# Kernel tuning notes

Measured on AMD Instinct MI355X. Metric: run time of the kernel, lower is better.

## Reference

```python
import jax, jax.numpy as jnp
import numpy as np


def setup_inputs() -> dict:
    key = jax.random.key(0)
    k1, k2 = jax.random.split(key)
    z = jax.random.normal(k1, (16, 128, 32, 32), dtype=jnp.float32)
    e = jax.random.normal(k2, (8192, 128), dtype=jnp.float32)
    log_sigma = jnp.zeros((1,), dtype=jnp.float32)  # init_log_sigma = 0.0
    return {"z": z, "e": e, "log_sigma": log_sigma}


def reference(z, e, log_sigma):
    # z: [B, C, H, W] latents; e: [M, C] codebook; log_sigma: [1]
    B, C, H, W = z.shape
    zf = jnp.transpose(z, (0, 2, 3, 1)).reshape(-1, C)  # [N, C]
    N = zf.shape[0]
    M = e.shape[0]
    T = 1.0  # latent_temp default

    # squared L2 distance via expanded dot products: ||z||^2 + ||e||^2 - 2 z.e
    z_sq = jnp.sum(zf * zf, axis=1, keepdims=True)          # [N, 1]
    e_sq = jnp.sum(e * e, axis=1)[None, :]                  # [1, M]
    dist = jnp.maximum(z_sq + e_sq - 2.0 * (zf @ e.T), 0.0)  # [N, M]

    alpha = -1.0 / (2.0 * jnp.exp(log_sigma[0]) ** 2)
    A = alpha * dist / T                                     # [N, M]

    # np.log(np.e) == 1.0 in the original
    const = 0.5 * C * (2.0 * log_sigma - 1.0)                # [1]
    lse1_loss = -jnp.mean(T * jax.nn.logsumexp(A, axis=1)) + const + jnp.log(float(M))
    lse2_loss = -jnp.mean(T * jax.nn.logsumexp(A, axis=0)) + const + jnp.log(float(N))
    return lse1_loss, lse2_loss
```

## Files before the change

### kernel.cpp

```cpp
#include <hip/hip_runtime.h>
#include <hip/hip_bf16.h>

typedef unsigned short u16;
typedef __attribute__((ext_vector_type(8))) short short8;
typedef __attribute__((ext_vector_type(4))) float float4v;

#define N_ROWS 16384
#define M_COLS 8192
#define KDIM   128
#define SHIFT  64.0f
#define STRIPES 64
#define SPLITS  32
#define CHUNKS  4

__device__ inline u16 f2bf(float f) {
  unsigned u = __builtin_bit_cast(unsigned, f);
  unsigned r = (u + 0x7fffu + ((u >> 16) & 1u)) >> 16;
  return (u16)r;
}

__global__ void prep(const float* __restrict__ z, const float* __restrict__ e,
                     u16* __restrict__ zf, u16* __restrict__ ef,
                     float* __restrict__ zsq, float* __restrict__ esq,
                     double* __restrict__ dacc, unsigned* __restrict__ dcnt) {
  if (blockIdx.x < 512) {
    const int b = blockIdx.x >> 5, h = blockIdx.x & 31;
    __shared__ float tile[128 * 33];
    __shared__ float psum[8][32];
    const float* src = z + ((size_t)b * 128 * 32 + h) * 32;
    for (int idx = threadIdx.x; idx < 4096; idx += 256) {
      int c = idx >> 5, w = idx & 31;
      tile[c * 33 + w] = src[c * 1024 + w];
    }
    __syncthreads();
    {
      int w = threadIdx.x & 31, cg = threadIdx.x >> 5;
      float s = 0.f;
#pragma unroll
      for (int cc = 0; cc < 16; ++cc) {
        float v = tile[(cg * 16 + cc) * 33 + w];
        s = fmaf(v, v, s);
      }
      psum[cg][w] = s;
    }
    for (int idx = threadIdx.x; idx < 512; idx += 256) {
      int w = idx >> 4, g = idx & 15;
      short8 v;
#pragma unroll
      for (int cc = 0; cc < 8; ++cc) v[cc] = (short)f2bf(tile[(g * 8 + cc) * 33 + w]);
      *(short8*)&zf[((size_t)b * 1024 + h * 32 + w) * 128 + g * 8] = v;
    }
    __syncthreads();
    if (threadIdx.x < 32) {
      int w = threadIdx.x;
      float s = 0.f;
#pragma unroll
      for (int cg = 0; cg < 8; ++cg) s += psum[cg][w];
      zsq[b * 1024 + h * 32 + w] = s;
    }
  } else {
    if (blockIdx.x == 512 && threadIdx.x == 0) {
      __hip_atomic_store(&dacc[0], 0.0, __ATOMIC_RELAXED, __HIP_MEMORY_SCOPE_AGENT);
      __hip_atomic_store(&dacc[1], 0.0, __ATOMIC_RELAXED, __HIP_MEMORY_SCOPE_AGENT);
      __hip_atomic_store(dcnt, 0u, __ATOMIC_RELAXED, __HIP_MEMORY_SCOPE_AGENT);
    }
    const int gw = ((blockIdx.x - 512) * 256 + threadIdx.x) >> 6;
    const int ln = threadIdx.x & 63;
    for (int r = gw; r < M_COLS; r += 512) {
      float2 v = *(const float2*)&e[r * 128 + ln * 2];
      unsigned pk = (unsigned)f2bf(v.x) | ((unsigned)f2bf(v.y) << 16);
      *(unsigned*)&ef[r * 128 + ln * 2] = pk;
      float s = fmaf(v.x, v.x, v.y * v.y);
#pragma unroll
      for (int sh = 1; sh < 64; sh <<= 1) s += __shfl_xor(s, sh);
      if (ln == 0) esq[r] = s;
    }
  }
}

__global__ __launch_bounds__(512, 4) void gemm_lse(
    const u16* __restrict__ zf, const u16* __restrict__ ef,
    const float* __restrict__ zsq, const float* __restrict__ esq,
    const float* __restrict__ log_sigma,
    float* __restrict__ rpart, float* __restrict__ cpart) {
  __shared__ __align__(16) u16 et[256 * 128];
  __shared__ float colacc[8][256];
  const int tid = threadIdx.x;
  const int ln = tid & 63, wv = tid >> 6;
  const int l15 = ln & 15, q = ln >> 4;
  const int stripe = blockIdx.x, split = blockIdx.y;
  const int colbase = split * 256;

  {
    const u16* efb = ef + (size_t)colbase * 128;
#pragma unroll
    for (int it = 0; it < 8; ++it) {
      int u = it * 512 + tid;
      int r = u >> 4, p_ = u & 15;
      int g = p_ ^ (r & 15);
      __builtin_amdgcn_global_load_lds(
          (const __attribute__((address_space(1))) unsigned int*)(efb + r * 128 + g * 8),
          (__attribute__((address_space(3))) unsigned int*)(et + (it * 512 + wv * 64) * 8),
          16, 0, 0);
    }
  }

  short8 af[2][4];
#pragma unroll
  for (int i = 0; i < 2; ++i)
#pragma unroll
    for (int kk = 0; kk < 4; ++kk)
      af[i][kk] = *(const short8*)(zf +
          (size_t)(stripe * 256 + wv * 32 + i * 16 + l15) * 128 + kk * 32 + q * 8);

  const float lsv = log_sigma[0];
  const float sg = __expf(lsv);
  const float alpha = -0.5f / (sg * sg);
  const float L2E = 1.44269504088896f;
  const float ca = alpha * L2E, cb = SHIFT * L2E, m2ca = -2.0f * ca;

  float4v zbl[2];
#pragma unroll
  for (int i = 0; i < 2; ++i) {
    float4v zs = *(const float4v*)(zsq + stripe * 256 + wv * 32 + i * 16 + q * 4);
#pragma unroll
    for (int r = 0; r < 4; ++r) zbl[i][r] = fmaf(ca, zs[r], cb);
  }

  float2 rs2[2][2];
#pragma unroll
  for (int i = 0; i < 2; ++i)
#pragma unroll
    for (int p = 0; p < 2; ++p) rs2[i][p] = make_float2(0.f, 0.f);

  __syncthreads();

#pragma unroll 1
  for (int t = 0; t < CHUNKS; ++t) {
    float ebv[4];
#pragma unroll
    for (int j = 0; j < 4; ++j) ebv[j] = ca * esq[colbase + t * 64 + j * 16 + l15];

    const u16* bb = et + t * 64 * 128;

    float4v acc[2][4];
#pragma unroll
    for (int kk = 0; kk < 4; ++kk) {
      short8 bfr[4];
      const int poff = ((kk * 4 + q) ^ l15) * 8;
#pragma unroll
      for (int j = 0; j < 4; ++j)
        bfr[j] = *(const short8*)(bb + (j * 16 + l15) * 128 + poff);
      if (kk == 0) {
#pragma unroll
        for (int i = 0; i < 2; ++i)
#pragma unroll
          for (int j = 0; j < 4; ++j)
            acc[i][j] = __builtin_amdgcn_mfma_f32_16x16x32_bf16(
                af[i][0], bfr[j], (float4v){0.f, 0.f, 0.f, 0.f}, 0, 0, 0);
      } else {
#pragma unroll
        for (int i = 0; i < 2; ++i)
#pragma unroll
          for (int j = 0; j < 4; ++j)
            acc[i][j] = __builtin_amdgcn_mfma_f32_16x16x32_bf16(
                af[i][kk], bfr[j], acc[i][j], 0, 0, 0);
      }
    }

    float2 cs2[4];
#pragma unroll
    for (int j = 0; j < 4; ++j) cs2[j] = make_float2(0.f, 0.f);

#pragma unroll
    for (int i = 0; i < 2; ++i) {
#pragma unroll
      for (int j = 0; j < 4; ++j) {
        float e0 = __builtin_amdgcn_exp2f(fmaf(acc[i][j][0], m2ca, zbl[i][0] + ebv[j]));
        float e1 = __builtin_amdgcn_exp2f(fmaf(acc[i][j][1], m2ca, zbl[i][1] + ebv[j]));
        float e2 = __builtin_amdgcn_exp2f(fmaf(acc[i][j][2], m2ca, zbl[i][2] + ebv[j]));
        float e3 = __builtin_amdgcn_exp2f(fmaf(acc[i][j][3], m2ca, zbl[i][3] + ebv[j]));
        rs2[i][0].x += e0; rs2[i][0].y += e1;
        rs2[i][1].x += e2; rs2[i][1].y += e3;
        cs2[j].x += e0 + e2; cs2[j].y += e1 + e3;
      }
    }
#pragma unroll
    for (int j = 0; j < 4; ++j) {
      float c = cs2[j].x + cs2[j].y;
      c += __shfl_xor(c, 16);
      c += __shfl_xor(c, 32);
      if (q == 0) colacc[wv][t * 64 + j * 16 + l15] = c;
    }
  }

  __syncthreads();
  if (tid < 256) {
    float s = 0.f;
#pragma unroll
    for (int w = 0; w < 8; ++w) s += colacc[w][tid];
    cpart[(size_t)stripe * M_COLS + colbase + tid] = s;
  }

#pragma unroll
  for (int i = 0; i < 2; ++i)
#pragma unroll
    for (int p = 0; p < 2; ++p)
      for (int s = 1; s < 16; s <<= 1) {
        rs2[i][p].x += __shfl_xor(rs2[i][p].x, s);
        rs2[i][p].y += __shfl_xor(rs2[i][p].y, s);
      }
  if (l15 == 0) {
#pragma unroll
    for (int i = 0; i < 2; ++i) {
      int rbase = stripe * 256 + wv * 32 + i * 16 + q * 4;
      rpart[(size_t)split * N_ROWS + rbase + 0] = rs2[i][0].x;
      rpart[(size_t)split * N_ROWS + rbase + 1] = rs2[i][0].y;
      rpart[(size_t)split * N_ROWS + rbase + 2] = rs2[i][1].x;
      rpart[(size_t)split * N_ROWS + rbase + 3] = rs2[i][1].y;
    }
  }
}

__global__ void fin(const float* __restrict__ rpart, const float* __restrict__ cpart,
                    const float* __restrict__ log_sigma,
                    double* __restrict__ dacc, unsigned* __restrict__ dcnt,
                    float* __restrict__ out) {
  const int tid = threadIdx.x, b = blockIdx.x;
  double v;
  if (b < 64) {
    int row = b * 256 + tid;
    float s = 0.f;
#pragma unroll
    for (int p = 0; p < SPLITS; ++p) s += rpart[(size_t)p * N_ROWS + row];
    v = (double)logf(s);
  } else {
    int col = (b - 64) * 256 + tid;
    float s = 0.f;
#pragma unroll
    for (int p = 0; p < STRIPES; ++p) s += cpart[(size_t)p * M_COLS + col];
    v = (double)logf(s);
  }
  __shared__ double red[256];
  red[tid] = v;
  __syncthreads();
  for (int s = 128; s > 0; s >>= 1) {
    if (tid < s) red[tid] += red[tid + s];
    __syncthreads();
  }
  if (tid == 0) {
    atomicAdd(&dacc[b < 64 ? 0 : 1], red[0]);
    __threadfence();
    unsigned ticket = atomicAdd(dcnt, 1u);
    if (ticket == 95u) {
      double s1 = atomicAdd(&dacc[0], 0.0);
      double s2 = atomicAdd(&dacc[1], 0.0);
      float lsv = log_sigma[0];
      float cst = 0.5f * 128.0f * (2.0f * lsv - 1.0f);
      out[0] = (float)(-(s1 / N_ROWS - (double)SHIFT)) + cst + logf((float)M_COLS);
      out[1] = (float)(-(s2 / M_COLS - (double)SHIFT)) + cst + logf((float)N_ROWS);
    }
  }
}

extern "C" void kernel_launch(void* const* d_in, const int* in_sizes, int n_in,
                              void* d_out, int out_size, void* d_ws, size_t ws_size,
                              hipStream_t stream) {
  const float* z  = (const float*)d_in[0];
  const float* e  = (const float*)d_in[1];
  const float* ls = (const float*)d_in[2];
  float* out = (float*)d_out;
  char* ws = (char*)d_ws;
  u16*   zf    = (u16*)ws;
  u16*   ef    = (u16*)(ws + (4u << 20));
  float* zsq   = (float*)(ws + (6u << 20));
  float* esq   = (float*)(ws + (6u << 20) + (64u << 10));
  float* rpart = (float*)(ws + (6u << 20) + (96u << 10));
  float* cpart = (float*)(ws + (8u << 20) + (96u << 10));
  double* dacc = (double*)(ws + (10u << 20) + (96u << 10));
  unsigned* dcnt = (unsigned*)(ws + (10u << 20) + (96u << 10) + 16);

  prep<<<dim3(640), dim3(256), 0, stream>>>(z, e, zf, ef, zsq, esq, dacc, dcnt);
  gemm_lse<<<dim3(STRIPES, SPLITS), dim3(512), 0, stream>>>(zf, ef, zsq, esq, ls, rpart, cpart);
  fin<<<dim3(96), dim3(256), 0, stream>>>(rpart, cpart, ls, dacc, dcnt, out);
}
```

Before: 143.5 us.

## Retile GEMM-LSE to 256x128 blocks with four waves and packed float2 epilogue

Halves the column tile per block (128 codebook entries) and doubles splits, using 256-thread blocks where each wave owns 64 rows and 32 columns per chunk, so each B fragment loaded from LDS feeds more MFMAs. Shared memory per block is halved, which allows more resident blocks. The exp epilogue is rewritten with two-wide float vectors so the compiler can emit packed FMA/add instructions. In exchange, row partials double in size, which adds traffic and work to the final reduction kernel, and the larger A fragment set raises register pressure.

```diff
diff --git a/kernel.cpp b/kernel.cpp
--- a/kernel.cpp
+++ b/kernel.cpp
@@ -4,13 +4,14 @@
 typedef unsigned short u16;
 typedef __attribute__((ext_vector_type(8))) short short8;
 typedef __attribute__((ext_vector_type(4))) float float4v;
+typedef __attribute__((ext_vector_type(2))) float float2v;
 
 #define N_ROWS 16384
 #define M_COLS 8192
 #define KDIM   128
 #define SHIFT  64.0f
 #define STRIPES 64
-#define SPLITS  32
+#define SPLITS  64
 #define CHUNKS  4
 
 __device__ inline u16 f2bf(float f) {
@@ -78,146 +79,151 @@
   }
 }
 
-__global__ __launch_bounds__(512, 4) void gemm_lse(
+__global__ __launch_bounds__(256, 3) void gemm_lse(
     const u16* __restrict__ zf, const u16* __restrict__ ef,
     const float* __restrict__ zsq, const float* __restrict__ esq,
     const float* __restrict__ log_sigma,
     float* __restrict__ rpart, float* __restrict__ cpart) {
-  __shared__ __align__(16) u16 et[256 * 128];
-  __shared__ float colacc[8][256];
+  __shared__ __align__(16) u16 et[128 * 128];
+  __shared__ float colacc[4][128];
   const int tid = threadIdx.x;
   const int ln = tid & 63, wv = tid >> 6;
   const int l15 = ln & 15, q = ln >> 4;
   const int stripe = blockIdx.x, split = blockIdx.y;
-  const int colbase = split * 256;
+  const int colbase = split * 128;
 
   {
     const u16* efb = ef + (size_t)colbase * 128;
 #pragma unroll
     for (int it = 0; it < 8; ++it) {
-      int u = it * 512 + tid;
+      int u = it * 256 + tid;
       int r = u >> 4, p_ = u & 15;
       int g = p_ ^ (r & 15);
       __builtin_amdgcn_global_load_lds(
           (const __attribute__((address_space(1))) unsigned int*)(efb + r * 128 + g * 8),
-          (__attribute__((address_space(3))) unsigned int*)(et + (it * 512 + wv * 64) * 8),
+          (__attribute__((address_space(3))) unsigned int*)(et + (it * 256 + wv * 64) * 8),
           16, 0, 0);
     }
   }
 
-  short8 af[2][4];
-#pragma unroll
-  for (int i = 0; i < 2; ++i)
+  short8 af[4][4];
+#pragma unroll
+  for (int i = 0; i < 4; ++i)
 #pragma unroll
     for (int kk = 0; kk < 4; ++kk)
       af[i][kk] = *(const short8*)(zf +
-          (size_t)(stripe * 256 + wv * 32 + i * 16 + l15) * 128 + kk * 32 + q * 8);
+          (size_t)(stripe * 256 + wv * 64 + i * 16 + l15) * 128 + kk * 32 + q * 8);
 
   const float lsv = log_sigma[0];
   const float sg = __expf(lsv);
   const float alpha = -0.5f / (sg * sg);
   const float L2E = 1.44269504088896f;
   const float ca = alpha * L2E, cb = SHIFT * L2E, m2ca = -2.0f * ca;
-
-  float4v zbl[2];
-#pragma unroll
-  for (int i = 0; i < 2; ++i) {
-    float4v zs = *(const float4v*)(zsq + stripe * 256 + wv * 32 + i * 16 + q * 4);
-#pragma unroll
-    for (int r = 0; r < 4; ++r) zbl[i][r] = fmaf(ca, zs[r], cb);
-  }
-
-  float2 rs2[2][2];
-#pragma unroll
-  for (int i = 0; i < 2; ++i)
-#pragma unroll
-    for (int p = 0; p < 2; ++p) rs2[i][p] = make_float2(0.f, 0.f);
+  const float2v m2ca2 = {m2ca, m2ca};
+
+  float2v zb2[4][2];
+#pragma unroll
+  for (int i = 0; i < 4; ++i) {
+    float4v zs = *(const float4v*)(zsq + stripe * 256 + wv * 64 + i * 16 + q * 4);
+    zb2[i][0] = (float2v){fmaf(ca, zs[0], cb), fmaf(ca, zs[1], cb)};
+    zb2[i][1] = (float2v){fmaf(ca, zs[2], cb), fmaf(ca, zs[3], cb)};
+  }
+
+  float2v rs01[4], rs23[4];
+#pragma unroll
+  for (int i = 0; i < 4; ++i) {
+    rs01[i] = (float2v){0.f, 0.f};
+    rs23[i] = (float2v){0.f, 0.f};
+  }
 
   __syncthreads();
 
 #pragma unroll 1
   for (int t = 0; t < CHUNKS; ++t) {
-    float ebv[4];
-#pragma unroll
-    for (int j = 0; j < 4; ++j) ebv[j] = ca * esq[colbase + t * 64 + j * 16 + l15];
-
-    const u16* bb = et + t * 64 * 128;
-
-    float4v acc[2][4];
+    float ebv[2];
+#pragma unroll
+    for (int j = 0; j < 2; ++j) ebv[j] = ca * esq[colbase + t * 32 + j * 16 + l15];
+
+    const u16* bb = et + t * 32 * 128;
+
+    float4v acc[4][2];
 #pragma unroll
     for (int kk = 0; kk < 4; ++kk) {
-      short8 bfr[4];
+      short8 bfr[2];
       const int poff = ((kk * 4 + q) ^ l15) * 8;
 #pragma unroll
-      for (int j = 0; j < 4; ++j)
+      for (int j = 0; j < 2; ++j)
         bfr[j] = *(const short8*)(bb + (j * 16 + l15) * 128 + poff);
       if (kk == 0) {
 #pragma unroll
-        for (int i = 0; i < 2; ++i)
-#pragma unroll
-          for (int j = 0; j < 4; ++j)
+        for (int i = 0; i < 4; ++i)
+#pragma unroll
+          for (int j = 0; j < 2; ++j)
             acc[i][j] = __builtin_amdgcn_mfma_f32_16x16x32_bf16(
                 af[i][0], bfr[j], (float4v){0.f, 0.f, 0.f, 0.f}, 0, 0, 0);
       } else {
 #pragma unroll
-        for (int i = 0; i < 2; ++i)
-#pragma unroll
-          for (int j = 0; j < 4; ++j)
+        for (int i = 0; i < 4; ++i)
+#pragma unroll
+          for (int j = 0; j < 2; ++j)
             acc[i][j] = __builtin_amdgcn_mfma_f32_16x16x32_bf16(
                 af[i][kk], bfr[j], acc[i][j], 0, 0, 0);
       }
     }
 
-    float2 cs2[4];
-#pragma unroll
-    for (int j = 0; j < 4; ++j) cs2[j] = make_float2(0.f, 0.f);
-
-#pragma unroll
-    for (int i = 0; i < 2; ++i) {
-#pragma unroll
-      for (int j = 0; j < 4; ++j) {
-        float e0 = __builtin_amdgcn_exp2f(fmaf(acc[i][j][0], m2ca, zbl[i][0] + ebv[j]));
-        float e1 = __builtin_amdgcn_exp2f(fmaf(acc[i][j][1], m2ca, zbl[i][1] + ebv[j]));
-        float e2 = __builtin_amdgcn_exp2f(fmaf(acc[i][j][2], m2ca, zbl[i][2] + ebv[j]));
-        float e3 = __builtin_amdgcn_exp2f(fmaf(acc[i][j][3], m2ca, zbl[i][3] + ebv[j]));
-        rs2[i][0].x += e0; rs2[i][0].y += e1;
-        rs2[i][1].x += e2; rs2[i][1].y += e3;
-        cs2[j].x += e0 + e2; cs2[j].y += e1 + e3;
+    float2v csv[2];
+    csv[0] = (float2v){0.f, 0.f};
+    csv[1] = (float2v){0.f, 0.f};
+
+#pragma unroll
+    for (int i = 0; i < 4; ++i) {
+#pragma unroll
+      for (int j = 0; j < 2; ++j) {
+        float2v eb2 = {ebv[j], ebv[j]};
+        float2v a01 = {acc[i][j][0], acc[i][j][1]};
+        float2v a23 = {acc[i][j][2], acc[i][j][3]};
+        float2v g01 = a01 * m2ca2 + (zb2[i][0] + eb2);
+        float2v g23 = a23 * m2ca2 + (zb2[i][1] + eb2);
+        float2v e01 = {__builtin_amdgcn_exp2f(g01.x), __builtin_amdgcn_exp2f(g01.y)};
+        float2v e23 = {__builtin_amdgcn_exp2f(g23.x), __builtin_amdgcn_exp2f(g23.y)};
+        rs01[i] += e01;
+        rs23[i] += e23;
+        csv[j] += e01 + e23;
       }
     }
 #pragma unroll
-    for (int j = 0; j < 4; ++j) {
-      float c = cs2[j].x + cs2[j].y;
+    for (int j = 0; j < 2; ++j) {
+      float c = csv[j].x + csv[j].y;
       c += __shfl_xor(c, 16);
       c += __shfl_xor(c, 32);
-      if (q == 0) colacc[wv][t * 64 + j * 16 + l15] = c;
+      if (q == 0) colacc[wv][t * 32 + j * 16 + l15] = c;
     }
   }
 
   __syncthreads();
-  if (tid < 256) {
+  if (tid < 128) {
     float s = 0.f;
 #pragma unroll
-    for (int w = 0; w < 8; ++w) s += colacc[w][tid];
+    for (int w = 0; w < 4; ++w) s += colacc[w][tid];
     cpart[(size_t)stripe * M_COLS + colbase + tid] = s;
   }
 
 #pragma unroll
-  for (int i = 0; i < 2; ++i)
-#pragma unroll
-    for (int p = 0; p < 2; ++p)
-      for (int s = 1; s < 16; s <<= 1) {
-        rs2[i][p].x += __shfl_xor(rs2[i][p].x, s);
-        rs2[i][p].y += __shfl_xor(rs2[i][p].y, s);
-      }
+  for (int i = 0; i < 4; ++i)
+    for (int s = 1; s < 16; s <<= 1) {
+      rs01[i].x += __shfl_xor(rs01[i].x, s);
+      rs01[i].y += __shfl_xor(rs01[i].y, s);
+      rs23[i].x += __shfl_xor(rs23[i].x, s);
+      rs23[i].y += __shfl_xor(rs23[i].y, s);
+    }
   if (l15 == 0) {
 #pragma unroll
-    for (int i = 0; i < 2; ++i) {
-      int rbase = stripe * 256 + wv * 32 + i * 16 + q * 4;
-      rpart[(size_t)split * N_ROWS + rbase + 0] = rs2[i][0].x;
-      rpart[(size_t)split * N_ROWS + rbase + 1] = rs2[i][0].y;
-      rpart[(size_t)split * N_ROWS + rbase + 2] = rs2[i][1].x;
-      rpart[(size_t)split * N_ROWS + rbase + 3] = rs2[i][1].y;
+    for (int i = 0; i < 4; ++i) {
+      int rbase = stripe * 256 + wv * 64 + i * 16 + q * 4;
+      rpart[(size_t)split * N_ROWS + rbase + 0] = rs01[i].x;
+      rpart[(size_t)split * N_ROWS + rbase + 1] = rs01[i].y;
+      rpart[(size_t)split * N_ROWS + rbase + 2] = rs23[i].x;
+      rpart[(size_t)split * N_ROWS + rbase + 3] = rs23[i].y;
     }
   }
 }
@@ -276,11 +282,11 @@
   float* zsq   = (float*)(ws + (6u << 20));
   float* esq   = (float*)(ws + (6u << 20) + (64u << 10));
   float* rpart = (float*)(ws + (6u << 20) + (96u << 10));
-  float* cpart = (float*)(ws + (8u << 20) + (96u << 10));
-  double* dacc = (double*)(ws + (10u << 20) + (96u << 10));
-  unsigned* dcnt = (unsigned*)(ws + (10u << 20) + (96u << 10) + 16);
+  float* cpart = (float*)(ws + (10u << 20) + (96u << 10));
+  double* dacc = (double*)(ws + (12u << 20) + (96u << 10));
+  unsigned* dcnt = (unsigned*)(ws + (12u << 20) + (96u << 10) + 16);
 
   prep<<<dim3(640), dim3(256), 0, stream>>>(z, e, zf, ef, zsq, esq, dacc, dcnt);
-  gemm_lse<<<dim3(STRIPES, SPLITS), dim3(512), 0, stream>>>(zf, ef, zsq, esq, ls, rpart, cpart);
+  gemm_lse<<<dim3(STRIPES, SPLITS), dim3(256), 0, stream>>>(zf, ef, zsq, esq, ls, rpart, cpart);
   fin<<<dim3(96), dim3(256), 0, stream>>>(rpart, cpart, ls, dacc, dcnt, out);
 }
```

New measurement: 153.9 us. 1.07x slower.
